# Optimization experiments

Measured on AMD Instinct MI355X. Metric: run time of the kernel, lower is better.

The kernel has to match this reference:

```python
import jax, jax.numpy as jnp
import numpy as np

B, N, E, F, H, OUT = 128, 2048, 16384, 32, 64, 16


def setup_inputs() -> dict:
    key = jax.random.key(0)
    ks = jax.random.split(key, 8)
    node_features = jax.random.normal(ks[0], (B, N, F), jnp.float32)
    edge_index = jax.random.randint(ks[1], (B, 2, E), 0, N)
    n_nodes = jax.random.randint(ks[2], (B,), N // 2, N + 1)
    # prefix node mask (required for the original's index-consistency)
    node_mask = jnp.arange(N)[None, :] < n_nodes[:, None]
    glorot = lambda k, sh, fan: jax.random.normal(k, sh, jnp.float32) / np.sqrt(fan)
    return dict(
        node_features=node_features, edge_index=edge_index, node_mask=node_mask,
        W1=glorot(ks[3], (F, H), F), b1=jnp.zeros((H,), jnp.float32),
        W2=glorot(ks[4], (H, H), H), b2=jnp.zeros((H,), jnp.float32),
        aW1=glorot(ks[5], (H, H), H), ab1=jnp.zeros((H,), jnp.float32),
        aW2=glorot(ks[6], (H, OUT), H), ab2=jnp.zeros((OUT,), jnp.float32),
    )


def reference(node_features, edge_index, node_mask, W1, b1, W2, b2, aW1, ab1, aW2, ab2):
    x = node_features
    src, dst = edge_index[:, 0], edge_index[:, 1]          # [B,E] source->target
    n = node_mask.sum(-1)                                   # [B] valid nodes per graph
    max_idx = n - 1
    emask = (src <= max_idx[:, None]) & (dst <= max_idx[:, None])
    w = emask.astype(x.dtype)                               # [B,E] edge weights

    # flatten batch into one big segment space [B*N]
    offs = (jnp.arange(B, dtype=src.dtype) * N)[:, None]
    src_f = (src + offs).reshape(-1)
    dst_f = (dst + offs).reshape(-1)
    w_f = w.reshape(-1)

    # GCN normalization with self-loops (PyG GCNConv default)
    deg = jax.ops.segment_sum(w_f, dst_f, num_segments=B * N).reshape(B, N)
    deg = deg + node_mask.astype(x.dtype)                   # self-loop weight 1 on valid nodes
    dis = jnp.where(deg > 0, jax.lax.rsqrt(deg), 0.0)       # deg^{-1/2}, [B,N]
    dis_f = dis.reshape(-1)
    norm = dis_f[src_f] * dis_f[dst_f] * w_f                # [B*E]
    nmask_f = node_mask.reshape(-1).astype(x.dtype)[:, None]
    nmask = node_mask.astype(x.dtype)[..., None]

    def gcn_relu(h, W, bias):
        hW = (h @ W).reshape(B * N, -1)                     # transform first (PyG order)
        msgs = hW[src_f] * norm[:, None]                    # [B*E, H]
        agg = jax.ops.segment_sum(msgs, dst_f, num_segments=B * N)
        agg = agg + hW * ((dis * dis).reshape(-1)[:, None] * nmask_f)  # self-loop term
        out = (agg.reshape(B, N, -1) + bias) * nmask
        return jax.nn.relu(out)

    h1 = gcn_relu(x * nmask, W1, b1)
    h2 = gcn_relu(h1, W2, b2)

    # mean pool over valid nodes (zeros if empty graph)
    pooled = h2.sum(1) / jnp.maximum(n, 1)[:, None].astype(x.dtype)
    hidden = jax.nn.relu(pooled @ aW1 + ab1)
    logits = hidden @ aW2 + ab2                             # [B, OUT]
    return logits
```

## Files before the change

kernel.cpp:

```cpp
#include <hip/hip_runtime.h>
#include <hip/hip_bf16.h>

#define B 128
#define N 2048
#define E 16384
#define F 32
#define H 64
#define OUTD 16
#define CAP 16
#define NP1 (N + 1)

typedef __attribute__((ext_vector_type(8))) short bf16x8;
typedef __attribute__((ext_vector_type(4))) float f32x4;

__device__ __forceinline__ float b2f(unsigned short u) {
    return __uint_as_float(((unsigned int)u) << 16);
}
__device__ __forceinline__ unsigned short f2b(float f) {
    unsigned int x = __float_as_uint(f);
    unsigned int r = (x + 0x7FFFu + ((x >> 16) & 1u)) >> 16;
    return (unsigned short)r;
}
__device__ __forceinline__ unsigned int pack2(float a, float b) {
    return (unsigned int)f2b(a) | ((unsigned int)f2b(b) << 16);
}

__device__ __forceinline__ void unpack8(float (&a)[8], uint4 u) {
    a[0] += __uint_as_float(u.x << 16);
    a[1] += __uint_as_float(u.x & 0xffff0000u);
    a[2] += __uint_as_float(u.y << 16);
    a[3] += __uint_as_float(u.y & 0xffff0000u);
    a[4] += __uint_as_float(u.z << 16);
    a[5] += __uint_as_float(u.z & 0xffff0000u);
    a[6] += __uint_as_float(u.w << 16);
    a[7] += __uint_as_float(u.w & 0xffff0000u);
}

struct PrepArgs {
    const void* src[9];
    void* dst[9];
};

__global__ __launch_bounds__(256) void k_prep(PrepArgs pa, int* flags) {
    const int bid = blockIdx.x;
    const int t = threadIdx.x;
    int sz;
    switch (bid) {
        case 0: sz = B * N * F; break;
        case 1: sz = F * H; break;
        case 2: sz = H; break;
        case 3: sz = H * H; break;
        case 4: sz = H; break;
        case 5: sz = H * H; break;
        case 6: sz = H; break;
        case 7: sz = H * OUTD; break;
        default: sz = OUTD; break;
    }
    const int K = sz < 1024 ? sz : 1024;
    const unsigned short* p = (const unsigned short*)pa.src[bid];
    float s = 0.f;
    for (int i = t; i < K; i += 256) s += fminf(fabsf(b2f(p[i])), 1e6f);
    __shared__ float red[256];
    __shared__ int isbf;
    red[t] = s;
    __syncthreads();
    for (int st = 128; st > 0; st >>= 1) {
        if (t < st) red[t] += red[t + st];
        __syncthreads();
    }
    if (t == 0) {
        int f = (red[0] < 100.0f * (float)K) ? 1 : 0;
        isbf = f;
        if (bid == 0) flags[0] = f;
    }
    __syncthreads();
    if (bid == 0) return;
    const int fl = isbf;
    auto rd = [&](int i) -> float {
        return fl ? b2f(((const unsigned short*)pa.src[bid])[i])
                  : ((const float*)pa.src[bid])[i];
    };
    if (bid == 1) {
        unsigned short* dst = (unsigned short*)pa.dst[bid];
        for (int i = t; i < F * H; i += 256) {
            int k = i >> 6, n2 = i & 63;
            dst[n2 * 40 + k] = f2b(rd(i));
        }
    } else if (bid == 3) {
        unsigned short* dst = (unsigned short*)pa.dst[bid];
        for (int i = t; i < H * H; i += 256) {
            int k = i >> 6, n2 = i & 63;
            dst[n2 * 72 + k] = f2b(rd(i));
        }
    } else {
        float* dst = (float*)pa.dst[bid];
        for (int i = t; i < sz; i += 256) dst[i] = rd(i);
    }
}

__global__ __launch_bounds__(1024) void k_build(
    const int* __restrict__ eidx, const void* __restrict__ mask,
    int* __restrict__ n_arr, float* __restrict__ dis,
    unsigned char* __restrict__ degc, unsigned short* __restrict__ ssrc,
    int2* __restrict__ ovf, int* __restrict__ ovf_cnt,
    float* __restrict__ pooled, unsigned int* __restrict__ y_u,
    unsigned int* __restrict__ z_u) {
    __shared__ int s_cnt[N];
    __shared__ int s_w[16];
    __shared__ int s_n;
    __shared__ int s_ovf;
    const int b = blockIdx.x;
    const int t = threadIdx.x;
    const int bN = b * N;
    const unsigned char* mb = (const unsigned char*)mask;
    int mode;
    if (mb[0] == 0x80 && mb[1] == 0x3F) mode = 2;
    else if (mb[0] != 0 && mb[1] != 0) mode = 0;
    else if (mb[0] != 0) mode = (mb[4] != 0) ? 1 : 4;
    else mode = 3;
    int cnt = 0;
    if (mode == 0) {
        const unsigned char* r = mb + (size_t)b * N;
        for (int i = t; i < N; i += 1024) cnt += (r[i] != 0);
    } else if (mode == 1 || mode == 3) {
        const unsigned int* r = (const unsigned int*)mask + (size_t)b * N;
        for (int i = t; i < N; i += 1024) cnt += (r[i] != 0);
    } else if (mode == 2) {
        const unsigned short* r = (const unsigned short*)mask + (size_t)b * N;
        for (int i = t; i < N; i += 1024) cnt += (r[i] != 0);
    } else {
        const unsigned long long* r = (const unsigned long long*)mask + (size_t)b * N;
        for (int i = t; i < N; i += 1024) cnt += (r[i] != 0ULL);
    }
    for (int o = 32; o > 0; o >>= 1) cnt += __shfl_down(cnt, o);
    if ((t & 63) == 0) s_w[t >> 6] = cnt;
    for (int i = t; i < N; i += 1024) s_cnt[i] = 0;
    if (t == 0) s_ovf = 0;
    __syncthreads();
    if (t == 0) {
        int a = 0;
        for (int i = 0; i < 16; i++) a += s_w[i];
        s_n = a > N ? N : a;
    }
    __syncthreads();
    const int n = s_n;
    const int4* es4 = (const int4*)(eidx + (size_t)b * 2 * E);
    const int4* ed4 = es4 + E / 4;
    for (int i = t; i < E / 4; i += 1024) {
        int4 s4 = es4[i], d4 = ed4[i];
        if ((unsigned)s4.x < (unsigned)n && (unsigned)d4.x < (unsigned)n) atomicAdd(&s_cnt[d4.x], 1);
        if ((unsigned)s4.y < (unsigned)n && (unsigned)d4.y < (unsigned)n) atomicAdd(&s_cnt[d4.y], 1);
        if ((unsigned)s4.z < (unsigned)n && (unsigned)d4.z < (unsigned)n) atomicAdd(&s_cnt[d4.z], 1);
        if ((unsigned)s4.w < (unsigned)n && (unsigned)d4.w < (unsigned)n) atomicAdd(&s_cnt[d4.w], 1);
    }
    {
        const int4 iv = make_int4(0x08000800, 0x08000800, 0x08000800, 0x08000800);
        int4* sp4 = (int4*)(ssrc + (size_t)bN * CAP);
        for (int i = t; i < N * CAP / 8; i += 1024) sp4[i] = iv;
    }
    if (t < 16) y_u[((size_t)b * NP1 + N) * (F / 2) + t] = 0u;
    if (t >= 32 && t < 64) z_u[((size_t)b * NP1 + N) * (H / 2) + (t - 32)] = 0u;
    __syncthreads();
    for (int v = t; v < N; v += 1024) {
        int c = s_cnt[v];
        dis[bN + v] = (v < n) ? rsqrtf((float)(c + 1)) : 0.0f;
        degc[bN + v] = (unsigned char)(c < CAP ? c : CAP);
        s_cnt[v] = 0;
    }
    __syncthreads();
    for (int i = t; i < E / 4; i += 1024) {
        int4 s4 = es4[i], d4 = ed4[i];
#define FILL1(SS, DD)                                                          \
        if ((unsigned)(SS) < (unsigned)n && (unsigned)(DD) < (unsigned)n) {    \
            int pos = atomicAdd(&s_cnt[DD], 1);                                \
            if (pos < CAP)                                                     \
                ssrc[((size_t)(bN + (DD))) * CAP + pos] = (unsigned short)(SS);\
            else {                                                             \
                int oi = atomicAdd(&s_ovf, 1);                                 \
                if (oi < E) ovf[(size_t)b * E + oi] = make_int2((DD), (SS));   \
            }                                                                  \
        }
        FILL1(s4.x, d4.x) FILL1(s4.y, d4.y) FILL1(s4.z, d4.z) FILL1(s4.w, d4.w)
#undef FILL1
    }
    if (t == 0) { n_arr[b] = n; ovf_cnt[b] = s_ovf; }
    if (t < H) pooled[b * H + t] = 0.0f;
}

__global__ __launch_bounds__(256) void k_premult(
    const void* __restrict__ x, const int* __restrict__ bf16flag,
    const float* __restrict__ dis, unsigned int* __restrict__ y_u) {
    const int gid = blockIdx.x * 256 + threadIdx.x;
    const int g = gid >> 4;
    const int f2 = gid & 15;
    const int b = g >> 11;
    const int v = g & (N - 1);
    const float dv = dis[g];
    float a, c;
    if (*bf16flag) {
        const unsigned short* xp = (const unsigned short*)x + (size_t)g * F + 2 * f2;
        a = b2f(xp[0]); c = b2f(xp[1]);
    } else {
        const float* xp = (const float*)x + (size_t)g * F + 2 * f2;
        a = xp[0]; c = xp[1];
    }
    y_u[((size_t)b * NP1 + v) * (F / 2) + f2] = pack2(a * dv, c * dv);
}

__global__ __launch_bounds__(256) void k_agg_gemm1(
    const unsigned int* __restrict__ y_u, const float* __restrict__ dis,
    const unsigned char* __restrict__ degc, const unsigned short* __restrict__ ssrc,
    const int2* __restrict__ ovf, const int* __restrict__ ovf_cnt,
    const unsigned short* __restrict__ w1t, const float* __restrict__ b1f,
    unsigned short* __restrict__ zs) {
    __shared__ unsigned short s_e[64 * CAP];
    __shared__ unsigned char s_dg[64];
    __shared__ float s_dv[64];
    __shared__ float s_b1[64];
    __shared__ __align__(16) unsigned short s_w1t[64 * 40];
    __shared__ __align__(16) unsigned short s_a1[64 * 40];
    const int bid = blockIdx.x;
    const int b = (bid & 7) + ((bid >> 8) << 3);
    const int v0 = ((bid >> 3) & 31) * 64;
    const int t = threadIdx.x;
    const int bN = b * N;
    if (t < 128) ((int4*)s_e)[t] = ((const int4*)(ssrc + (size_t)(bN + v0) * CAP))[t];
    if (t >= 128 && t < 144)
        ((unsigned int*)s_dg)[t - 128] = ((const unsigned int*)(degc + bN + v0))[t - 128];
    if (t >= 192) s_dv[t - 192] = dis[bN + v0 + (t - 192)];
    if (t >= 144 && t < 208) s_b1[t - 144] = b1f[t - 144];
    for (int i = t; i < 320; i += 256) ((int4*)s_w1t)[i] = ((const int4*)w1t)[i];
    __syncthreads();
    const int lane = t & 63;
    const int w = t >> 6;
    const int oc = ovf_cnt[b];
    const unsigned int* yb = y_u + (size_t)b * NP1 * (F / 2);
    {
        const int nn = w * 16 + (lane >> 2);
        const int v = v0 + nn;
        const int cu = (lane & 3) * 4;
        int md = s_dg[w * 16 + (lane & 15)];
        int m2;
        m2 = __shfl_xor(md, 1); md = md > m2 ? md : m2;
        m2 = __shfl_xor(md, 2); md = md > m2 ? md : m2;
        m2 = __shfl_xor(md, 4); md = md > m2 ? md : m2;
        m2 = __shfl_xor(md, 8); md = md > m2 ? md : m2;
        const unsigned short* ep = &s_e[nn * CAP];
        float a[8] = {0.f, 0.f, 0.f, 0.f, 0.f, 0.f, 0.f, 0.f};
        uint4 cur = *(const uint4*)(yb + (size_t)v * (F / 2) + cu);
        uint4 nxt = *(const uint4*)(yb + (size_t)ep[0] * (F / 2) + cu);
        for (int s = 0; s < md; s++) {
            int sn = s + 1; sn = sn > CAP - 1 ? CAP - 1 : sn;
            uint4 n2 = *(const uint4*)(yb + (size_t)ep[sn] * (F / 2) + cu);
            unpack8(a, cur);
            cur = nxt; nxt = n2;
        }
        unpack8(a, cur);
        if (oc > 0) {
            const int2* ob = ovf + (size_t)b * E;
            for (int j = 0; j < oc; j++) {
                int2 o = ob[j];
                if (o.x == v) {
                    uint4 u4 = *(const uint4*)(yb + (size_t)o.y * (F / 2) + cu);
                    unpack8(a, u4);
                }
            }
        }
        const float dv = s_dv[nn];
        uint4 ov;
        ov.x = pack2(a[0] * dv, a[1] * dv);
        ov.y = pack2(a[2] * dv, a[3] * dv);
        ov.z = pack2(a[4] * dv, a[5] * dv);
        ov.w = pack2(a[6] * dv, a[7] * dv);
        *(uint4*)((unsigned int*)s_a1 + nn * 20 + cu) = ov;
    }
    __syncthreads();
    const int quad = lane >> 4;
    const int f2 = lane & 15;
    const int m0 = w * 16;
    bf16x8 af = *(const bf16x8*)&s_a1[(m0 + f2) * 40 + quad * 8];
    float dvr[4];
#pragma unroll
    for (int r = 0; r < 4; r++) dvr[r] = s_dv[m0 + quad * 4 + r];
#pragma unroll
    for (int nt = 0; nt < 4; nt++) {
        bf16x8 bf = *(const bf16x8*)&s_w1t[(nt * 16 + f2) * 40 + quad * 8];
        f32x4 acc = {0.f, 0.f, 0.f, 0.f};
        acc = __builtin_amdgcn_mfma_f32_16x16x32_bf16(af, bf, acc, 0, 0, 0);
        float bb = s_b1[nt * 16 + f2];
#pragma unroll
        for (int r = 0; r < 4; r++) {
            int row = m0 + quad * 4 + r;
            float val = dvr[r] * fmaxf(acc[r] + bb, 0.0f);
            zs[((size_t)b * NP1 + v0 + row) * H + nt * 16 + f2] = f2b(val);
        }
    }
}

__global__ __launch_bounds__(256) void k_agg_gemm2_pool(
    const unsigned int* __restrict__ z_u, const float* __restrict__ dis,
    const unsigned char* __restrict__ degc, const unsigned short* __restrict__ ssrc,
    const int2* __restrict__ ovf, const int* __restrict__ ovf_cnt,
    const unsigned short* __restrict__ w2t, const float* __restrict__ b2f_,
    float* __restrict__ pooled) {
    __shared__ unsigned short s_e[64 * CAP];
    __shared__ unsigned char s_dg[64];
    __shared__ float s_dv[64];
    __shared__ float s_b2[64];
    __shared__ __align__(16) unsigned short s_w2t[64 * 72];
    __shared__ __align__(16) unsigned short s_a2[64 * 72];
    __shared__ float s_pool[4][64];
    const int bid = blockIdx.x;
    const int b = (bid & 7) + ((bid >> 8) << 3);
    const int v0 = ((bid >> 3) & 31) * 64;
    const int t = threadIdx.x;
    const int bN = b * N;
    if (t < 128) ((int4*)s_e)[t] = ((const int4*)(ssrc + (size_t)(bN + v0) * CAP))[t];
    if (t >= 128 && t < 144)
        ((unsigned int*)s_dg)[t - 128] = ((const unsigned int*)(degc + bN + v0))[t - 128];
    if (t >= 192) s_dv[t - 192] = dis[bN + v0 + (t - 192)];
    if (t >= 144 && t < 208) s_b2[t - 144] = b2f_[t - 144];
    for (int i = t; i < 576; i += 256) ((int4*)s_w2t)[i] = ((const int4*)w2t)[i];
    __syncthreads();
    const int lane = t & 63;
    const int w = t >> 6;
    const int oc = ovf_cnt[b];
    const unsigned int* zb = z_u + (size_t)b * NP1 * (H / 2);
#pragma unroll
    for (int g = 0; g < 2; g++) {
        const int nn = w * 16 + g * 8 + (lane >> 3);
        const int v = v0 + nn;
        const int cu = (lane & 7) * 4;
        int md = s_dg[w * 16 + g * 8 + (lane & 7)];
        int m2;
        m2 = __shfl_xor(md, 1); md = md > m2 ? md : m2;
        m2 = __shfl_xor(md, 2); md = md > m2 ? md : m2;
        m2 = __shfl_xor(md, 4); md = md > m2 ? md : m2;
        const unsigned short* ep = &s_e[nn * CAP];
        float a[8] = {0.f, 0.f, 0.f, 0.f, 0.f, 0.f, 0.f, 0.f};
        uint4 cur = *(const uint4*)(zb + (size_t)v * (H / 2) + cu);
        uint4 nxt = *(const uint4*)(zb + (size_t)ep[0] * (H / 2) + cu);
        for (int s = 0; s < md; s++) {
            int sn = s + 1; sn = sn > CAP - 1 ? CAP - 1 : sn;
            uint4 n2 = *(const uint4*)(zb + (size_t)ep[sn] * (H / 2) + cu);
            unpack8(a, cur);
            cur = nxt; nxt = n2;
        }
        unpack8(a, cur);
        if (oc > 0) {
            const int2* ob = ovf + (size_t)b * E;
            for (int j = 0; j < oc; j++) {
                int2 o = ob[j];
                if (o.x == v) {
                    uint4 u4 = *(const uint4*)(zb + (size_t)o.y * (H / 2) + cu);
                    unpack8(a, u4);
                }
            }
        }
        const float dv = s_dv[nn];
        uint4 ov;
        ov.x = pack2(a[0] * dv, a[1] * dv);
        ov.y = pack2(a[2] * dv, a[3] * dv);
        ov.z = pack2(a[4] * dv, a[5] * dv);
        ov.w = pack2(a[6] * dv, a[7] * dv);
        *(uint4*)((unsigned int*)s_a2 + nn * 36 + cu) = ov;
    }
    __syncthreads();
    const int quad = lane >> 4;
    const int f2 = lane & 15;
    const int m0 = w * 16;
    bf16x8 af0 = *(const bf16x8*)&s_a2[(m0 + f2) * 72 + quad * 8];
    bf16x8 af1 = *(const bf16x8*)&s_a2[(m0 + f2) * 72 + 32 + quad * 8];
    float dvr[4];
#pragma unroll
    for (int r = 0; r < 4; r++) dvr[r] = s_dv[m0 + quad * 4 + r];
#pragma unroll
    for (int nt = 0; nt < 4; nt++) {
        bf16x8 bf0 = *(const bf16x8*)&s_w2t[(nt * 16 + f2) * 72 + quad * 8];
        bf16x8 bf1 = *(const bf16x8*)&s_w2t[(nt * 16 + f2) * 72 + 32 + quad * 8];
        f32x4 acc = {0.f, 0.f, 0.f, 0.f};
        acc = __builtin_amdgcn_mfma_f32_16x16x32_bf16(af0, bf0, acc, 0, 0, 0);
        acc = __builtin_amdgcn_mfma_f32_16x16x32_bf16(af1, bf1, acc, 0, 0, 0);
        float bb = s_b2[nt * 16 + f2];
        float ps = 0.f;
#pragma unroll
        for (int r = 0; r < 4; r++)
            ps += (dvr[r] > 0.0f) ? fmaxf(acc[r] + bb, 0.0f) : 0.0f;
        ps += __shfl_xor(ps, 16);
        ps += __shfl_xor(ps, 32);
        if (quad == 0) s_pool[w][nt * 16 + f2] = ps;
    }
    __syncthreads();
    if (t < H)
        atomicAdd(&pooled[b * H + t],
                  s_pool[0][t] + s_pool[1][t] + s_pool[2][t] + s_pool[3][t]);
}

__global__ __launch_bounds__(64) void k_mlp(
    const float* __restrict__ pooled, const int* __restrict__ n_arr,
    const float* __restrict__ aW1, const float* __restrict__ ab1,
    const float* __restrict__ aW2, const float* __restrict__ ab2,
    const int* __restrict__ flags, void* __restrict__ out) {
    const int b = blockIdx.x;
    const int t = threadIdx.x;
    __shared__ float p[64];
    __shared__ float hid[64];
    int n = n_arr[b];
    if (n < 1) n = 1;
    p[t] = pooled[b * H + t] / (float)n;
    __syncthreads();
    float acc = ab1[t];
    for (int j = 0; j < 64; j++) acc += p[j] * aW1[j * 64 + t];
    hid[t] = fmaxf(acc, 0.0f);
    __syncthreads();
    if (t < 16) {
        float a2 = ab2[t];
        for (int j = 0; j < 64; j++) a2 += hid[j] * aW2[j * 16 + t];
        if (flags[0]) ((unsigned short*)out)[b * OUTD + t] = f2b(a2);
        else          ((float*)out)[b * OUTD + t] = a2;
    }
}

extern "C" void kernel_launch(void* const* d_in, const int* in_sizes, int n_in,
                              void* d_out, int out_size, void* d_ws, size_t ws_size,
                              hipStream_t stream) {
    const void* x    = d_in[0];
    const int*  eidx = (const int*)d_in[1];
    const void* mask = d_in[2];

    char* ws = (char*)d_ws;
    size_t off = 0;
    auto alloc = [&](size_t bytes) -> void* {
        void* p = ws + off;
        off += (bytes + 255) & ~(size_t)255;
        return p;
    };
    int*   flags   = (int*)alloc(16 * sizeof(int));
    unsigned short* w1t = (unsigned short*)alloc(64 * 40 * 2);
    unsigned short* w2t = (unsigned short*)alloc(64 * 72 * 2);
    float* b1f     = (float*)alloc(H * sizeof(float));
    float* b2f_    = (float*)alloc(H * sizeof(float));
    float* aW1f    = (float*)alloc(H * H * sizeof(float));
    float* ab1f    = (float*)alloc(H * sizeof(float));
    float* aW2f    = (float*)alloc(H * OUTD * sizeof(float));
    float* ab2f    = (float*)alloc(OUTD * sizeof(float));
    int*   n_arr   = (int*)alloc(B * sizeof(int));
    float* dis     = (float*)alloc((size_t)B * N * sizeof(float));
    unsigned char*  degc = (unsigned char*)alloc((size_t)B * N);
    unsigned short* ssrc = (unsigned short*)alloc((size_t)B * N * CAP * 2);
    int2*  ovf     = (int2*)alloc((size_t)B * E * sizeof(int2));
    int*   ovf_cnt = (int*)alloc(B * sizeof(int));
    float* pooled  = (float*)alloc((size_t)B * H * sizeof(float));
    unsigned int* y_u = (unsigned int*)alloc((size_t)B * NP1 * (F / 2) * 4);
    unsigned int* z_u = (unsigned int*)alloc((size_t)B * NP1 * (H / 2) * 4);

    PrepArgs pa;
    pa.src[0] = x;        pa.dst[0] = pooled;
    pa.src[1] = d_in[3];  pa.dst[1] = w1t;
    pa.src[2] = d_in[4];  pa.dst[2] = b1f;
    pa.src[3] = d_in[5];  pa.dst[3] = w2t;
    pa.src[4] = d_in[6];  pa.dst[4] = b2f_;
    pa.src[5] = d_in[7];  pa.dst[5] = aW1f;
    pa.src[6] = d_in[8];  pa.dst[6] = ab1f;
    pa.src[7] = d_in[9];  pa.dst[7] = aW2f;
    pa.src[8] = d_in[10]; pa.dst[8] = ab2f;

    k_prep<<<9, 256, 0, stream>>>(pa, flags);
    k_build<<<B, 1024, 0, stream>>>(eidx, mask, n_arr, dis, degc, ssrc, ovf,
                                    ovf_cnt, pooled, y_u, z_u);
    k_premult<<<(B * N * (F / 2)) / 256, 256, 0, stream>>>(x, flags, dis, y_u);
    k_agg_gemm1<<<B * 32, 256, 0, stream>>>(y_u, dis, degc, ssrc, ovf, ovf_cnt,
                                            w1t, b1f, (unsigned short*)z_u);
    k_agg_gemm2_pool<<<B * 32, 256, 0, stream>>>(z_u, dis, degc, ssrc, ovf,
                                                 ovf_cnt, w2t, b2f_, pooled);
    k_mlp<<<B, 64, 0, stream>>>(pooled, n_arr, aW1f, ab1f, aW2f, ab2f, flags, d_out);
}
```

Baseline: 173.9 us.

## Fuse prep and premult into build kernel, drop separate degree-count pass

Folds the dtype-detection/weight-prep kernel and the dis-premultiply kernel into the per-graph build kernel, so three launches become one. The separate degree-counting pass over edges is removed; the fill pass's atomic slot counters now double as the degree counts. The x premultiply is vectorized per block with dis recomputed from shared counts. This cuts launch overhead and one edge read pass, but puts the premultiply on only 128 blocks instead of a wide grid.

```diff
diff --git a/kernel.cpp b/kernel.cpp
--- a/kernel.cpp
+++ b/kernel.cpp
@@ -41,77 +41,35 @@
     void* dst[9];
 };
 
-__global__ __launch_bounds__(256) void k_prep(PrepArgs pa, int* flags) {
-    const int bid = blockIdx.x;
-    const int t = threadIdx.x;
-    int sz;
-    switch (bid) {
-        case 0: sz = B * N * F; break;
-        case 1: sz = F * H; break;
-        case 2: sz = H; break;
-        case 3: sz = H * H; break;
-        case 4: sz = H; break;
-        case 5: sz = H * H; break;
-        case 6: sz = H; break;
-        case 7: sz = H * OUTD; break;
-        default: sz = OUTD; break;
-    }
-    const int K = sz < 1024 ? sz : 1024;
-    const unsigned short* p = (const unsigned short*)pa.src[bid];
-    float s = 0.f;
-    for (int i = t; i < K; i += 256) s += fminf(fabsf(b2f(p[i])), 1e6f);
-    __shared__ float red[256];
-    __shared__ int isbf;
-    red[t] = s;
-    __syncthreads();
-    for (int st = 128; st > 0; st >>= 1) {
-        if (t < st) red[t] += red[t + st];
-        __syncthreads();
-    }
-    if (t == 0) {
-        int f = (red[0] < 100.0f * (float)K) ? 1 : 0;
-        isbf = f;
-        if (bid == 0) flags[0] = f;
-    }
-    __syncthreads();
-    if (bid == 0) return;
-    const int fl = isbf;
-    auto rd = [&](int i) -> float {
-        return fl ? b2f(((const unsigned short*)pa.src[bid])[i])
-                  : ((const float*)pa.src[bid])[i];
-    };
-    if (bid == 1) {
-        unsigned short* dst = (unsigned short*)pa.dst[bid];
-        for (int i = t; i < F * H; i += 256) {
-            int k = i >> 6, n2 = i & 63;
-            dst[n2 * 40 + k] = f2b(rd(i));
-        }
-    } else if (bid == 3) {
-        unsigned short* dst = (unsigned short*)pa.dst[bid];
-        for (int i = t; i < H * H; i += 256) {
-            int k = i >> 6, n2 = i & 63;
-            dst[n2 * 72 + k] = f2b(rd(i));
-        }
-    } else {
-        float* dst = (float*)pa.dst[bid];
-        for (int i = t; i < sz; i += 256) dst[i] = rd(i);
-    }
-}
-
 __global__ __launch_bounds__(1024) void k_build(
-    const int* __restrict__ eidx, const void* __restrict__ mask,
+    const void* __restrict__ x, const int* __restrict__ eidx,
+    const void* __restrict__ mask, PrepArgs pa, int* __restrict__ flags,
     int* __restrict__ n_arr, float* __restrict__ dis,
     unsigned char* __restrict__ degc, unsigned short* __restrict__ ssrc,
     int2* __restrict__ ovf, int* __restrict__ ovf_cnt,
     float* __restrict__ pooled, unsigned int* __restrict__ y_u,
     unsigned int* __restrict__ z_u) {
     __shared__ int s_cnt[N];
+    __shared__ float s_fred[16];
     __shared__ int s_w[16];
-    __shared__ int s_n;
-    __shared__ int s_ovf;
+    __shared__ int s_n, s_ovf, s_xbf, s_pf;
     const int b = blockIdx.x;
     const int t = threadIdx.x;
     const int bN = b * N;
+    {
+        const unsigned short* p = (const unsigned short*)x;
+        float s = fminf(fabsf(b2f(p[t])), 1e6f);
+        for (int o = 32; o > 0; o >>= 1) s += __shfl_down(s, o);
+        if ((t & 63) == 0) s_fred[t >> 6] = s;
+        __syncthreads();
+        if (t == 0) {
+            float a = 0.f;
+            for (int i = 0; i < 16; i++) a += s_fred[i];
+            int f = (a < 100.0f * 1024.0f) ? 1 : 0;
+            s_xbf = f;
+            if (b == 0) flags[0] = f;
+        }
+    }
     const unsigned char* mb = (const unsigned char*)mask;
     int mode;
     if (mb[0] == 0x80 && mb[1] == 0x3F) mode = 2;
@@ -135,6 +93,13 @@
     for (int o = 32; o > 0; o >>= 1) cnt += __shfl_down(cnt, o);
     if ((t & 63) == 0) s_w[t >> 6] = cnt;
     for (int i = t; i < N; i += 1024) s_cnt[i] = 0;
+    {
+        const int4 iv = make_int4(0x08000800, 0x08000800, 0x08000800, 0x08000800);
+        int4* sp4 = (int4*)(ssrc + (size_t)bN * CAP);
+        for (int i = t; i < N * CAP / 8; i += 1024) sp4[i] = iv;
+    }
+    if (t < 16) y_u[((size_t)b * NP1 + N) * (F / 2) + t] = 0u;
+    if (t >= 32 && t < 64) z_u[((size_t)b * NP1 + N) * (H / 2) + (t - 32)] = 0u;
     if (t == 0) s_ovf = 0;
     __syncthreads();
     if (t == 0) {
@@ -146,28 +111,6 @@
     const int n = s_n;
     const int4* es4 = (const int4*)(eidx + (size_t)b * 2 * E);
     const int4* ed4 = es4 + E / 4;
-    for (int i = t; i < E / 4; i += 1024) {
-        int4 s4 = es4[i], d4 = ed4[i];
-        if ((unsigned)s4.x < (unsigned)n && (unsigned)d4.x < (unsigned)n) atomicAdd(&s_cnt[d4.x], 1);
-        if ((unsigned)s4.y < (unsigned)n && (unsigned)d4.y < (unsigned)n) atomicAdd(&s_cnt[d4.y], 1);
-        if ((unsigned)s4.z < (unsigned)n && (unsigned)d4.z < (unsigned)n) atomicAdd(&s_cnt[d4.z], 1);
-        if ((unsigned)s4.w < (unsigned)n && (unsigned)d4.w < (unsigned)n) atomicAdd(&s_cnt[d4.w], 1);
-    }
-    {
-        const int4 iv = make_int4(0x08000800, 0x08000800, 0x08000800, 0x08000800);
-        int4* sp4 = (int4*)(ssrc + (size_t)bN * CAP);
-        for (int i = t; i < N * CAP / 8; i += 1024) sp4[i] = iv;
-    }
-    if (t < 16) y_u[((size_t)b * NP1 + N) * (F / 2) + t] = 0u;
-    if (t >= 32 && t < 64) z_u[((size_t)b * NP1 + N) * (H / 2) + (t - 32)] = 0u;
-    __syncthreads();
-    for (int v = t; v < N; v += 1024) {
-        int c = s_cnt[v];
-        dis[bN + v] = (v < n) ? rsqrtf((float)(c + 1)) : 0.0f;
-        degc[bN + v] = (unsigned char)(c < CAP ? c : CAP);
-        s_cnt[v] = 0;
-    }
-    __syncthreads();
     for (int i = t; i < E / 4; i += 1024) {
         int4 s4 = es4[i], d4 = ed4[i];
 #define FILL1(SS, DD)                                                          \
@@ -183,28 +126,90 @@
         FILL1(s4.x, d4.x) FILL1(s4.y, d4.y) FILL1(s4.z, d4.z) FILL1(s4.w, d4.w)
 #undef FILL1
     }
+    __syncthreads();
+    for (int v = t; v < N; v += 1024) {
+        int c = s_cnt[v];
+        dis[bN + v] = (v < n) ? rsqrtf((float)(c + 1)) : 0.0f;
+        degc[bN + v] = (unsigned char)(c < CAP ? c : CAP);
+    }
+    if (t < H) pooled[b * H + t] = 0.0f;
     if (t == 0) { n_arr[b] = n; ovf_cnt[b] = s_ovf; }
-    if (t < H) pooled[b * H + t] = 0.0f;
-}
-
-__global__ __launch_bounds__(256) void k_premult(
-    const void* __restrict__ x, const int* __restrict__ bf16flag,
-    const float* __restrict__ dis, unsigned int* __restrict__ y_u) {
-    const int gid = blockIdx.x * 256 + threadIdx.x;
-    const int g = gid >> 4;
-    const int f2 = gid & 15;
-    const int b = g >> 11;
-    const int v = g & (N - 1);
-    const float dv = dis[g];
-    float a, c;
-    if (*bf16flag) {
-        const unsigned short* xp = (const unsigned short*)x + (size_t)g * F + 2 * f2;
-        a = b2f(xp[0]); c = b2f(xp[1]);
+    if (s_xbf) {
+        const uint4* xp = (const uint4*)((const unsigned short*)x + (size_t)bN * F);
+        for (int i = t; i < N * 4; i += 1024) {
+            const int v = i >> 2;
+            const int c = s_cnt[v];
+            const float dv = (v < n) ? rsqrtf((float)(c + 1)) : 0.0f;
+            uint4 u = xp[i];
+            uint4 o;
+            o.x = pack2(b2f((unsigned short)u.x) * dv, b2f((unsigned short)(u.x >> 16)) * dv);
+            o.y = pack2(b2f((unsigned short)u.y) * dv, b2f((unsigned short)(u.y >> 16)) * dv);
+            o.z = pack2(b2f((unsigned short)u.z) * dv, b2f((unsigned short)(u.z >> 16)) * dv);
+            o.w = pack2(b2f((unsigned short)u.w) * dv, b2f((unsigned short)(u.w >> 16)) * dv);
+            *(uint4*)(y_u + ((size_t)b * NP1 + v) * (F / 2) + (i & 3) * 4) = o;
+        }
     } else {
-        const float* xp = (const float*)x + (size_t)g * F + 2 * f2;
-        a = xp[0]; c = xp[1];
-    }
-    y_u[((size_t)b * NP1 + v) * (F / 2) + f2] = pack2(a * dv, c * dv);
+        const float4* xp = (const float4*)((const float*)x + (size_t)bN * F);
+        for (int i = t; i < N * 4; i += 1024) {
+            const int v = i >> 2;
+            const int c = s_cnt[v];
+            const float dv = (v < n) ? rsqrtf((float)(c + 1)) : 0.0f;
+            float4 v1 = xp[i * 2], v2 = xp[i * 2 + 1];
+            uint4 o;
+            o.x = pack2(v1.x * dv, v1.y * dv);
+            o.y = pack2(v1.z * dv, v1.w * dv);
+            o.z = pack2(v2.x * dv, v2.y * dv);
+            o.w = pack2(v2.z * dv, v2.w * dv);
+            *(uint4*)(y_u + ((size_t)b * NP1 + v) * (F / 2) + (i & 3) * 4) = o;
+        }
+    }
+    if (b >= 1 && b <= 8) {
+        int sz;
+        switch (b) {
+            case 1: sz = F * H; break;
+            case 2: sz = H; break;
+            case 3: sz = H * H; break;
+            case 4: sz = H; break;
+            case 5: sz = H * H; break;
+            case 6: sz = H; break;
+            case 7: sz = H * OUTD; break;
+            default: sz = OUTD; break;
+        }
+        const int K = sz < 1024 ? sz : 1024;
+        const unsigned short* p = (const unsigned short*)pa.src[b];
+        float s = (t < K) ? fminf(fabsf(b2f(p[t])), 1e6f) : 0.f;
+        for (int o = 32; o > 0; o >>= 1) s += __shfl_down(s, o);
+        __syncthreads();
+        if ((t & 63) == 0) s_fred[t >> 6] = s;
+        __syncthreads();
+        if (t == 0) {
+            float a = 0.f;
+            for (int i = 0; i < 16; i++) a += s_fred[i];
+            s_pf = (a < 100.0f * (float)K) ? 1 : 0;
+        }
+        __syncthreads();
+        const int fl = s_pf;
+        auto rd = [&](int i) -> float {
+            return fl ? b2f(((const unsigned short*)pa.src[b])[i])
+                      : ((const float*)pa.src[b])[i];
+        };
+        if (b == 1) {
+            unsigned short* dst = (unsigned short*)pa.dst[b];
+            for (int i = t; i < F * H; i += 1024) {
+                int k = i >> 6, n2 = i & 63;
+                dst[n2 * 40 + k] = f2b(rd(i));
+            }
+        } else if (b == 3) {
+            unsigned short* dst = (unsigned short*)pa.dst[b];
+            for (int i = t; i < H * H; i += 1024) {
+                int k = i >> 6, n2 = i & 63;
+                dst[n2 * 72 + k] = f2b(rd(i));
+            }
+        } else {
+            float* dst = (float*)pa.dst[b];
+            for (int i = t; i < sz; i += 1024) dst[i] = rd(i);
+        }
+    }
 }
 
 __global__ __launch_bounds__(256) void k_agg_gemm1(
@@ -465,10 +470,8 @@
     pa.src[7] = d_in[9];  pa.dst[7] = aW2f;
     pa.src[8] = d_in[10]; pa.dst[8] = ab2f;
 
-    k_prep<<<9, 256, 0, stream>>>(pa, flags);
-    k_build<<<B, 1024, 0, stream>>>(eidx, mask, n_arr, dis, degc, ssrc, ovf,
-                                    ovf_cnt, pooled, y_u, z_u);
-    k_premult<<<(B * N * (F / 2)) / 256, 256, 0, stream>>>(x, flags, dis, y_u);
+    k_build<<<B, 1024, 0, stream>>>(x, eidx, mask, pa, flags, n_arr, dis, degc,
+                                    ssrc, ovf, ovf_cnt, pooled, y_u, z_u);
     k_agg_gemm1<<<B * 32, 256, 0, stream>>>(y_u, dis, degc, ssrc, ovf, ovf_cnt,
                                             w1t, b1f, (unsigned short*)z_u);
     k_agg_gemm2_pool<<<B * 32, 256, 0, stream>>>(z_u, dis, degc, ssrc, ovf,
```

Measured after the change: 165.0 us (median of 2 runs). 5.1% less time.
